# Performance work log

Hardware: AMD Instinct MI355X
Metric: run time of the kernel (lower is better)

Reference implementation:

```python
import jax, jax.numpy as jnp
import numpy as np
from jax import lax

T = 16        # in_length
E = 32        # input_embedding_size_d
H = 64        # encoder_size
NG = 32       # vehicles per scene group
G = 1024      # number of scene groups
N = G * NG    # total vehicles
C = 3         # class_num

leaky = lambda x: jax.nn.leaky_relu(x, 0.1)

def _gru_final(x_seq, Wih, Whh, bih, bhh):
    # x_seq: (T, N, E). PyTorch GRU gate order: r, z, n. Returns final hidden (N, H).
    def step(h, x):
        gx = x @ Wih.T + bih
        gh = h @ Whh.T + bhh
        xr, xz, xn = jnp.split(gx, 3, axis=-1)
        hr, hz, hn = jnp.split(gh, 3, axis=-1)
        r = jax.nn.sigmoid(xr + hr)
        z = jax.nn.sigmoid(xz + hz)
        ng = jnp.tanh(xn + r * hn)
        return (1.0 - z) * ng + z * h, None
    h0 = jnp.zeros((x_seq.shape[1], Whh.shape[1]), x_seq.dtype)
    hT, _ = lax.scan(step, h0, x_seq)
    return hT

def setup_inputs() -> dict:
    key = jax.random.key(0)
    ks = jax.random.split(key, 24)
    def rn(k, shape, fan):
        return jax.random.normal(k, shape, jnp.float32) * np.float32(1.0 / np.sqrt(fan))
    inp = {}
    inp["scene"] = jax.random.normal(ks[0], (N, 2 * T), jnp.float32)
    inp["condition"] = jax.random.randint(ks[1], (N,), 0, C, jnp.int32)
    inp["hero_pos_index"] = jax.random.randint(ks[2], (G,), 0, N, jnp.int32)
    inp["nbrs_pos_index"] = jax.random.randint(ks[3], (N,), 0, N, jnp.int32)
    inp["index_div"] = jnp.arange(N, dtype=jnp.int32).reshape(G, NG)
    # ip_emb_d: Linear(2, E)
    inp["W_emb"] = rn(ks[4], (2, E), 2)
    inp["b_emb"] = jnp.zeros((E,), jnp.float32)
    # forward / backward GRUs (weight_ih: (3H,E), weight_hh: (3H,H))
    inp["Wih_f"] = rn(ks[5], (3 * H, E), E); inp["Whh_f"] = rn(ks[6], (3 * H, H), H)
    inp["bih_f"] = jnp.zeros((3 * H,), jnp.float32); inp["bhh_f"] = jnp.zeros((3 * H,), jnp.float32)
    inp["Wih_b"] = rn(ks[7], (3 * H, E), E); inp["Whh_b"] = rn(ks[8], (3 * H, H), H)
    inp["bih_b"] = jnp.zeros((3 * H,), jnp.float32); inp["bhh_b"] = jnp.zeros((3 * H,), jnp.float32)
    # mlp: Linear(H, H//2)
    inp["Wm"] = rn(ks[9], (H, H // 2), H); inp["bm"] = jnp.zeros((H // 2,), jnp.float32)
    # spatial_mlp: Linear(2T, H) -> Linear(H, H//2)
    inp["Ws1"] = rn(ks[10], (2 * T, H), 2 * T); inp["bs1"] = jnp.zeros((H,), jnp.float32)
    inp["Ws2"] = rn(ks[11], (H, H // 2), H); inp["bs2"] = jnp.zeros((H // 2,), jnp.float32)
    # op_d: Linear(H, H//4) -> Linear(H//4, C)
    inp["Wo1"] = rn(ks[12], (H, H // 4), H); inp["bo1"] = jnp.zeros((H // 4,), jnp.float32)
    inp["Wo2"] = rn(ks[13], (H // 4, C), H // 4); inp["bo2"] = jnp.zeros((C,), jnp.float32)
    return inp

def reference(scene, condition, hero_pos_index, nbrs_pos_index, index_div,
              W_emb, b_emb, Wih_f, Whh_f, bih_f, bhh_f, Wih_b, Whh_b, bih_b, bhh_b,
              Wm, bm, Ws1, bs1, Ws2, bs2, Wo1, bo1, Wo2, bo2):
    n_total = scene.shape[0]
    # scene.view(-1,2,T).permute(2,0,1) -> (T, N, 2)
    scene_t = scene.reshape(n_total, 2, T).transpose(2, 0, 1)
    emb = leaky(scene_t @ W_emb + b_emb)                 # (T, N, E)
    h_f = _gru_final(emb, Wih_f, Whh_f, bih_f, bhh_f)    # (N, H)
    h_b = _gru_final(emb[::-1], Wih_b, Whh_b, bih_b, bhh_b)
    seq_enc = leaky(((h_f + h_b) * 0.5) @ Wm + bm)       # (N, H//2)
    # pairwise relative features within each group: rel[g, j, i] = x_i - x_j
    feat_g = scene[index_div]                            # (G, n, 2T); row layout == permute(1,2,0).view(-1,2T)
    rel = feat_g[:, None, :, :] - feat_g[:, :, None, :]  # (G, n, n, 2T)
    enc = leaky(leaky(rel @ Ws1 + bs1) @ Ws2 + bs2)      # (G, n, n, H//2)
    # diagonal pairs (i==j) are dropped in the original; subtract mlp(0) then divide by n-1
    zero_enc = leaky(leaky(bs1) @ Ws2 + bs2)             # (H//2,)
    n_grp = index_div.shape[1]
    pooled = (enc.sum(axis=2) - zero_enc) / (n_grp - 1)  # (G, n, H//2)
    pooled = pooled.reshape(n_total, -1)                 # group-concat order == vehicle order (arange groups)
    full_enc = jnp.concatenate([seq_enc, pooled], axis=1)  # (N, H)
    x_logit = leaky(full_enc @ Wo1 + bo1) @ Wo2 + bo2      # (N, C)
    return x_logit, full_enc
```

## Files before the change

### kernel.cpp

```cpp
#include <hip/hip_runtime.h>
#include <hip/hip_bf16.h>

#define TT 16
#define EE 32
#define HH 64
#define NGRP 32
#define CC 3

typedef __attribute__((ext_vector_type(8))) short short8;
typedef __attribute__((ext_vector_type(4))) float floatx4;

#define MFMA16(a, b, c) __builtin_amdgcn_mfma_f32_16x16x32_bf16((a), (b), (c), 0, 0, 0)

__device__ __forceinline__ float leakyf(float x) { return fmaxf(x, 0.1f * x); }
__device__ __forceinline__ float sigmoidf_fast(float x) {
    return __builtin_amdgcn_rcpf(1.0f + __expf(-x));
}
__device__ __forceinline__ float tanhf_fast(float x) {
    return 1.0f - 2.0f * __builtin_amdgcn_rcpf(__expf(2.0f * x) + 1.0f);
}
__device__ __forceinline__ short f2bf(float x) {
    unsigned u = __float_as_uint(x);
    return (short)((u + 0x7FFFu + ((u >> 16) & 1u)) >> 16);
}
__device__ __forceinline__ float bf2f(short s) {
    return __uint_as_float(((unsigned)(unsigned short)s) << 16);
}
__device__ __forceinline__ short8 ld8bf(const float* __restrict__ p) {
    const float4 a = *(const float4*)p;
    const float4 b = *(const float4*)(p + 4);
    short8 v;
    v[0] = f2bf(a.x); v[1] = f2bf(a.y); v[2] = f2bf(a.z); v[3] = f2bf(a.w);
    v[4] = f2bf(b.x); v[5] = f2bf(b.y); v[6] = f2bf(b.z); v[7] = f2bf(b.w);
    return v;
}

__global__ __launch_bounds__(512, 6) void gru_mfma_kernel(
    const float* __restrict__ scene,
    const float* __restrict__ W_emb, const float* __restrict__ b_emb,
    const float* __restrict__ Wih_f, const float* __restrict__ Whh_f,
    const float* __restrict__ bih_f, const float* __restrict__ bhh_f,
    const float* __restrict__ Wih_b, const float* __restrict__ Whh_b,
    const float* __restrict__ bih_b, const float* __restrict__ bhh_b,
    const float* __restrict__ Wm, const float* __restrict__ bm,
    float* __restrict__ full_enc)
{
    __shared__ __align__(16) short Xall[16 * 2 * 64 * 8];
    __shared__ __align__(16) short Hf[2 * 2 * 2 * 64 * 8];

    const int tid  = threadIdx.x;
    const int lane = tid & 63;
    const int w    = __builtin_amdgcn_readfirstlane(tid >> 6);
    const int dir  = w >> 2;
    const int wd   = w & 3;
    const int cc   = lane & 15;
    const int quad = lane >> 4;
    const int vbase = blockIdx.x * 32;
    const int j    = wd * 16 + cc;
    const int ks_w = j >> 5;
    const int qa_w = (j >> 3) & 3;
    const int ii_w = j & 7;

    {
        const int t   = tid >> 5;
        const int veh = tid & 31;
        const int n   = vbase + veh;
        const float xs = scene[n * 32 + t];
        const float ys = scene[n * 32 + 16 + t];
        const int mt = veh >> 4;
        const int m  = veh & 15;
        #pragma unroll
        for (int q = 0; q < 4; ++q) {
            short8 v;
            #pragma unroll
            for (int i2 = 0; i2 < 8; ++i2) {
                const int e = q * 8 + i2;
                v[i2] = f2bf(leakyf(fmaf(xs, W_emb[e], fmaf(ys, W_emb[EE + e], b_emb[e]))));
            }
            *(short8*)&Xall[(((t * 2 + mt) * 64) + q * 16 + m) * 8] = v;
        }
        const short8 z8 = {0, 0, 0, 0, 0, 0, 0, 0};
        *(short8*)&Hf[tid * 8] = z8;
    }

    const float* Wih = dir ? Wih_b : Wih_f;
    const float* Whh = dir ? Whh_b : Whh_f;
    const float* bih = dir ? bih_b : bih_f;
    const float* bhh = dir ? bhh_b : bhh_f;
    const int k0 = quad * 8;
    const short8 Br0  = ld8bf(Whh + (j      ) * 64 + k0);
    const short8 Br1  = ld8bf(Whh + (j      ) * 64 + 32 + k0);
    const short8 Br2  = ld8bf(Wih + (j      ) * 32 + k0);
    const short8 Bz0  = ld8bf(Whh + (j +  64) * 64 + k0);
    const short8 Bz1  = ld8bf(Whh + (j +  64) * 64 + 32 + k0);
    const short8 Bz2  = ld8bf(Wih + (j +  64) * 32 + k0);
    const short8 Bhn0 = ld8bf(Whh + (j + 128) * 64 + k0);
    const short8 Bhn1 = ld8bf(Whh + (j + 128) * 64 + 32 + k0);
    const short8 Bxn  = ld8bf(Wih + (j + 128) * 32 + k0);
    const float b_r  = bih[j] + bhh[j];
    const float b_z  = bih[j + 64] + bhh[j + 64];
    const float b_xn = bih[j + 128];
    const float b_hn = bhh[j + 128];

    float h_reg[8];
    #pragma unroll
    for (int i = 0; i < 8; ++i) h_reg[i] = 0.0f;

    short* HfD = &Hf[dir * (2 * 2 * 64 * 8)];
    __syncthreads();

    #pragma unroll 1
    for (int s = 0; s < TT; ++s) {
        const int t = dir ? (TT - 1 - s) : s;
        #pragma unroll
        for (int mt = 0; mt < 2; ++mt) {
            const short8 Ah0 = *(const short8*)&HfD[((0 * 2 + mt) * 64 + lane) * 8];
            const short8 Ah1 = *(const short8*)&HfD[((1 * 2 + mt) * 64 + lane) * 8];
            const short8 Axx = *(const short8*)&Xall[((t * 2 + mt) * 64 + lane) * 8];
            const floatx4 z4 = {0.f, 0.f, 0.f, 0.f};
            const floatx4 ar  = MFMA16(Axx, Br2, MFMA16(Ah1, Br1, MFMA16(Ah0, Br0, z4)));
            const floatx4 az  = MFMA16(Axx, Bz2, MFMA16(Ah1, Bz1, MFMA16(Ah0, Bz0, z4)));
            const floatx4 ahn = MFMA16(Ah1, Bhn1, MFMA16(Ah0, Bhn0, z4));
            const floatx4 axn = MFMA16(Axx, Bxn, z4);
            #pragma unroll
            for (int r = 0; r < 4; ++r) {
                const float rr = sigmoidf_fast(ar[r] + b_r);
                const float zz = sigmoidf_fast(az[r] + b_z);
                const float ng = tanhf_fast(fmaf(rr, ahn[r] + b_hn, axn[r] + b_xn));
                const float h0 = h_reg[mt * 4 + r];
                h_reg[mt * 4 + r] = fmaf(zz, h0 - ng, ng);
            }
        }
        __syncthreads();
        #pragma unroll
        for (int mt = 0; mt < 2; ++mt) {
            #pragma unroll
            for (int r = 0; r < 4; ++r) {
                const int la = qa_w * 16 + (quad * 4 + r);
                HfD[((ks_w * 2 + mt) * 64 + la) * 8 + ii_w] = f2bf(h_reg[mt * 4 + r]);
            }
        }
        __syncthreads();
    }

    if (w < 4) {
        const int nt   = w >> 1;
        const int mt_e = w & 1;
        const int n_col = nt * 16 + cc;
        short8 Bm0, Bm1;
        #pragma unroll
        for (int i = 0; i < 8; ++i) {
            Bm0[i] = f2bf(Wm[(     quad * 8 + i) * 32 + n_col]);
            Bm1[i] = f2bf(Wm[(32 + quad * 8 + i) * 32 + n_col]);
        }
        short8 A0, A1;
        #pragma unroll
        for (int ks = 0; ks < 2; ++ks) {
            const short8 F = *(const short8*)&Hf[(((0 * 2 + ks) * 2 + mt_e) * 64 + lane) * 8];
            const short8 B = *(const short8*)&Hf[(((1 * 2 + ks) * 2 + mt_e) * 64 + lane) * 8];
            #pragma unroll
            for (int i = 0; i < 8; ++i) {
                const short v = f2bf(0.5f * (bf2f(F[i]) + bf2f(B[i])));
                if (ks == 0) A0[i] = v; else A1[i] = v;
            }
        }
        const floatx4 z4 = {0.f, 0.f, 0.f, 0.f};
        const floatx4 acc = MFMA16(A1, Bm1, MFMA16(A0, Bm0, z4));
        const float bmn = bm[n_col];
        #pragma unroll
        for (int r = 0; r < 4; ++r) {
            const int veh = mt_e * 16 + quad * 4 + r;
            full_enc[(vbase + veh) * HH + n_col] = leakyf(acc[r] + bmn);
        }
    }
}

__global__ __launch_bounds__(256, 4) void spatial_mfma_kernel(
    const float* __restrict__ scene, const int* __restrict__ index_div,
    const float* __restrict__ Ws1, const float* __restrict__ bs1,
    const float* __restrict__ Ws2, const float* __restrict__ bs2,
    float* __restrict__ full_enc)
{
    __shared__ float sfeat[NGRP][33];
    __shared__ float su[NGRP][68];
    __shared__ float szero[32];

    const int g    = blockIdx.x;
    const int tid  = threadIdx.x;
    const int lane = tid & 63;
    const int w    = __builtin_amdgcn_readfirstlane(tid >> 6);
    const int cc   = lane & 15;
    const int quad = lane >> 4;

    {
        const int v  = tid >> 3;
        const int c0 = (tid & 7) * 4;
        const int n  = index_div[g * NGRP + v];
        const float4 f4 = *(const float4*)(scene + n * (2 * TT) + c0);
        sfeat[v][c0 + 0] = f4.x; sfeat[v][c0 + 1] = f4.y;
        sfeat[v][c0 + 2] = f4.z; sfeat[v][c0 + 3] = f4.w;
    }
    __syncthreads();

    {
        const int v  = tid >> 3;
        const int d0 = (tid & 7) * 8;
        float acc[8];
        #pragma unroll
        for (int i = 0; i < 8; ++i) acc[i] = 0.0f;
        #pragma unroll
        for (int e = 0; e < EE; ++e) {
            const float f = sfeat[v][e];
            const float4 w0 = *(const float4*)&Ws1[e * 64 + d0];
            const float4 w1 = *(const float4*)&Ws1[e * 64 + d0 + 4];
            acc[0] = fmaf(f, w0.x, acc[0]); acc[1] = fmaf(f, w0.y, acc[1]);
            acc[2] = fmaf(f, w0.z, acc[2]); acc[3] = fmaf(f, w0.w, acc[3]);
            acc[4] = fmaf(f, w1.x, acc[4]); acc[5] = fmaf(f, w1.y, acc[5]);
            acc[6] = fmaf(f, w1.z, acc[6]); acc[7] = fmaf(f, w1.w, acc[7]);
        }
        #pragma unroll
        for (int i = 0; i < 8; ++i) su[v][d0 + i] = acc[i];
    }
    if (tid < 32) {
        float zs = bs2[tid];
        #pragma unroll
        for (int d = 0; d < HH; ++d) zs = fmaf(leakyf(bs1[d]), Ws2[d * 32 + tid], zs);
        szero[tid] = leakyf(zs);
    }

    short8 Bw00, Bw01, Bw10, Bw11;
    #pragma unroll
    for (int i = 0; i < 8; ++i) {
        Bw00[i] = f2bf(Ws2[(     quad * 8 + i) * 32 + cc]);
        Bw01[i] = f2bf(Ws2[(32 + quad * 8 + i) * 32 + cc]);
        Bw10[i] = f2bf(Ws2[(     quad * 8 + i) * 32 + 16 + cc]);
        Bw11[i] = f2bf(Ws2[(32 + quad * 8 + i) * 32 + 16 + cc]);
    }
    float bsq0[8], bsq1[8];
    #pragma unroll
    for (int i = 0; i < 8; ++i) {
        bsq0[i] = bs1[quad * 8 + i];
        bsq1[i] = bs1[32 + quad * 8 + i];
    }
    const float bs2c0 = bs2[cc], bs2c1 = bs2[16 + cc];
    __syncthreads();

    #pragma unroll 2
    for (int jj = 0; jj < 8; ++jj) {
        const int jrow = w * 8 + jj;
        float vj0[8], vj1[8];
        #pragma unroll
        for (int i = 0; i < 8; ++i) {
            vj0[i] = su[jrow][quad * 8 + i] - bsq0[i];
            vj1[i] = su[jrow][32 + quad * 8 + i] - bsq1[i];
        }
        float acc0 = 0.0f, acc1 = 0.0f;
        #pragma unroll
        for (int it = 0; it < 2; ++it) {
            const int irow = it * 16 + cc;
            const float4 p0 = *(const float4*)&su[irow][quad * 8];
            const float4 p1 = *(const float4*)&su[irow][quad * 8 + 4];
            const float4 p2 = *(const float4*)&su[irow][32 + quad * 8];
            const float4 p3 = *(const float4*)&su[irow][32 + quad * 8 + 4];
            short8 A0, A1;
            A0[0] = f2bf(leakyf(p0.x - vj0[0])); A0[1] = f2bf(leakyf(p0.y - vj0[1]));
            A0[2] = f2bf(leakyf(p0.z - vj0[2])); A0[3] = f2bf(leakyf(p0.w - vj0[3]));
            A0[4] = f2bf(leakyf(p1.x - vj0[4])); A0[5] = f2bf(leakyf(p1.y - vj0[5]));
            A0[6] = f2bf(leakyf(p1.z - vj0[6])); A0[7] = f2bf(leakyf(p1.w - vj0[7]));
            A1[0] = f2bf(leakyf(p2.x - vj1[0])); A1[1] = f2bf(leakyf(p2.y - vj1[1]));
            A1[2] = f2bf(leakyf(p2.z - vj1[2])); A1[3] = f2bf(leakyf(p2.w - vj1[3]));
            A1[4] = f2bf(leakyf(p3.x - vj1[4])); A1[5] = f2bf(leakyf(p3.y - vj1[5]));
            A1[6] = f2bf(leakyf(p3.z - vj1[6])); A1[7] = f2bf(leakyf(p3.w - vj1[7]));
            const floatx4 z4 = {0.f, 0.f, 0.f, 0.f};
            const floatx4 D0 = MFMA16(A1, Bw01, MFMA16(A0, Bw00, z4));
            const floatx4 D1 = MFMA16(A1, Bw11, MFMA16(A0, Bw10, z4));
            #pragma unroll
            for (int r = 0; r < 4; ++r) {
                acc0 += leakyf(D0[r] + bs2c0);
                acc1 += leakyf(D1[r] + bs2c1);
            }
        }
        acc0 += __shfl_xor(acc0, 16, 64); acc0 += __shfl_xor(acc0, 32, 64);
        acc1 += __shfl_xor(acc1, 16, 64); acc1 += __shfl_xor(acc1, 32, 64);
        const int row = g * NGRP + jrow;
        if (quad == 0)
            full_enc[row * HH + 32 + cc] = (acc0 - szero[cc]) * (1.0f / 31.0f);
        else if (quad == 1)
            full_enc[row * HH + 48 + cc] = (acc1 - szero[16 + cc]) * (1.0f / 31.0f);
    }
}

__global__ __launch_bounds__(64) void head_kernel(
    const float* __restrict__ full_enc,
    const float* __restrict__ Wo1, const float* __restrict__ bo1,
    const float* __restrict__ Wo2, const float* __restrict__ bo2,
    float* __restrict__ out)
{
    const int n = blockIdx.x * 64 + threadIdx.x;
    float t1[16];
    #pragma unroll
    for (int m = 0; m < 16; ++m) t1[m] = bo1[m];
    const float4* fe4 = (const float4*)(full_enc + n * HH);
    #pragma unroll
    for (int k4 = 0; k4 < 16; ++k4) {
        const float4 f = fe4[k4];
        const float fv[4] = {f.x, f.y, f.z, f.w};
        #pragma unroll
        for (int u = 0; u < 4; ++u) {
            const int k = k4 * 4 + u;
            #pragma unroll
            for (int m = 0; m < 16; ++m) t1[m] = fmaf(fv[u], Wo1[k * 16 + m], t1[m]);
        }
    }
    float l0 = bo2[0], l1 = bo2[1], l2 = bo2[2];
    #pragma unroll
    for (int m = 0; m < 16; ++m) {
        const float a = leakyf(t1[m]);
        l0 = fmaf(a, Wo2[m * 3 + 0], l0);
        l1 = fmaf(a, Wo2[m * 3 + 1], l1);
        l2 = fmaf(a, Wo2[m * 3 + 2], l2);
    }
    out[n * 3 + 0] = l0;
    out[n * 3 + 1] = l1;
    out[n * 3 + 2] = l2;
}

extern "C" void kernel_launch(void* const* d_in, const int* in_sizes, int n_in,
                              void* d_out, int out_size, void* d_ws, size_t ws_size,
                              hipStream_t stream) {
    const float* scene     = (const float*)d_in[0];
    const int*   index_div = (const int*)d_in[4];
    const float* W_emb = (const float*)d_in[5];
    const float* b_emb = (const float*)d_in[6];
    const float* Wih_f = (const float*)d_in[7];
    const float* Whh_f = (const float*)d_in[8];
    const float* bih_f = (const float*)d_in[9];
    const float* bhh_f = (const float*)d_in[10];
    const float* Wih_b = (const float*)d_in[11];
    const float* Whh_b = (const float*)d_in[12];
    const float* bih_b = (const float*)d_in[13];
    const float* bhh_b = (const float*)d_in[14];
    const float* Wm  = (const float*)d_in[15];
    const float* bm  = (const float*)d_in[16];
    const float* Ws1 = (const float*)d_in[17];
    const float* bs1 = (const float*)d_in[18];
    const float* Ws2 = (const float*)d_in[19];
    const float* bs2 = (const float*)d_in[20];
    const float* Wo1 = (const float*)d_in[21];
    const float* bo1 = (const float*)d_in[22];
    const float* Wo2 = (const float*)d_in[23];
    const float* bo2 = (const float*)d_in[24];

    const int N = in_sizes[0] / (2 * TT);
    const int G = in_sizes[4] / NGRP;

    float* out      = (float*)d_out;
    float* full_enc = out + (size_t)N * CC;

    gru_mfma_kernel<<<dim3(N / 32), dim3(512), 0, stream>>>(
        scene, W_emb, b_emb, Wih_f, Whh_f, bih_f, bhh_f,
        Wih_b, Whh_b, bih_b, bhh_b, Wm, bm, full_enc);

    spatial_mfma_kernel<<<dim3(G), dim3(256), 0, stream>>>(
        scene, index_div, Ws1, bs1, Ws2, bs2, full_enc);

    head_kernel<<<dim3(N / 64), dim3(64), 0, stream>>>(
        full_enc, Wo1, bo1, Wo2, bo2, out);
}
```

Baseline: 226.3 us.

## Double-buffer GRU state, compute embeddings per step, fuse head into spatial kernel

The GRU kernel now computes each timestep's input embedding on the fly into a double-buffered LDS tile and ping-pongs the hidden-state buffer, so each step needs one barrier instead of two. It also folds the gate biases into the MFMA accumulator init and uses cheaper round-half-up bf16 conversion. The output head is fused into the spatial kernel, which reads the GRU half of full_enc and keeps the pooled half in LDS, removing a launch and a global round trip. The risks are higher LDS use per block and changed bf16 rounding. The spatial kernel also assumes that group g covers contiguous vehicles g*32 to g*32+31 (arange index_div).

```diff
diff --git a/kernel.cpp b/kernel.cpp
--- a/kernel.cpp
+++ b/kernel.cpp
@@ -8,6 +8,7 @@
 #define CC 3
 
 typedef __attribute__((ext_vector_type(8))) short short8;
+typedef __attribute__((ext_vector_type(4))) short short4v;
 typedef __attribute__((ext_vector_type(4))) float floatx4;
 
 #define MFMA16(a, b, c) __builtin_amdgcn_mfma_f32_16x16x32_bf16((a), (b), (c), 0, 0, 0)
@@ -22,6 +23,9 @@
 __device__ __forceinline__ short f2bf(float x) {
     unsigned u = __float_as_uint(x);
     return (short)((u + 0x7FFFu + ((u >> 16) & 1u)) >> 16);
+}
+__device__ __forceinline__ short f2bf_h(float x) {
+    return (short)((__float_as_uint(x) + 0x8000u) >> 16);
 }
 __device__ __forceinline__ float bf2f(short s) {
     return __uint_as_float(((unsigned)(unsigned short)s) << 16);
@@ -45,8 +49,9 @@
     const float* __restrict__ Wm, const float* __restrict__ bm,
     float* __restrict__ full_enc)
 {
-    __shared__ __align__(16) short Xall[16 * 2 * 64 * 8];
-    __shared__ __align__(16) short Hf[2 * 2 * 2 * 64 * 8];
+    __shared__ float sscene[32][33];
+    __shared__ __align__(16) short Xb[2 * 2 * 2 * 64 * 8];
+    __shared__ __align__(16) short Hf[2 * 2 * 2 * 2 * 64 * 8];
 
     const int tid  = threadIdx.x;
     const int lane = tid & 63;
@@ -61,26 +66,41 @@
     const int qa_w = (j >> 3) & 3;
     const int ii_w = j & 7;
 
+    for (int idx = tid; idx < 1024; idx += 512) {
+        const int v = idx >> 5, c = idx & 31;
+        sscene[c][v] = scene[(vbase + v) * 32 + c];
+    }
     {
-        const int t   = tid >> 5;
-        const int veh = tid & 31;
-        const int n   = vbase + veh;
-        const float xs = scene[n * 32 + t];
-        const float ys = scene[n * 32 + 16 + t];
-        const int mt = veh >> 4;
-        const int m  = veh & 15;
-        #pragma unroll
-        for (int q = 0; q < 4; ++q) {
-            short8 v;
-            #pragma unroll
-            for (int i2 = 0; i2 < 8; ++i2) {
-                const int e = q * 8 + i2;
-                v[i2] = f2bf(leakyf(fmaf(xs, W_emb[e], fmaf(ys, W_emb[EE + e], b_emb[e]))));
-            }
-            *(short8*)&Xall[(((t * 2 + mt) * 64) + q * 16 + m) * 8] = v;
-        }
         const short8 z8 = {0, 0, 0, 0, 0, 0, 0, 0};
-        *(short8*)&Hf[tid * 8] = z8;
+        *(short8*)&Hf[(tid >> 8) * 4096 + (tid & 255) * 8] = z8;
+    }
+
+    const int l     = tid & 255;
+    const int veh_x = l & 31;
+    const int q2    = l >> 5;
+    const int e0    = q2 * 4;
+    const int mtx   = veh_x >> 4;
+    const int mx    = veh_x & 15;
+    const int chx   = e0 >> 3;
+    const int i0x   = e0 & 7;
+    float w0e[4], w1e[4], bbe[4];
+    #pragma unroll
+    for (int d = 0; d < 4; ++d) {
+        w0e[d] = W_emb[e0 + d];
+        w1e[d] = W_emb[EE + e0 + d];
+        bbe[d] = b_emb[e0 + d];
+    }
+    const int xoff = dir * 2048 + (mtx * 64 + chx * 16 + mx) * 8 + i0x;
+
+    {
+        const int t0 = dir ? (TT - 1) : 0;
+        const float xs = sscene[t0][veh_x];
+        const float ys = sscene[16 + t0][veh_x];
+        short4v v;
+        #pragma unroll
+        for (int d = 0; d < 4; ++d)
+            v[d] = f2bf_h(leakyf(fmaf(xs, w0e[d], fmaf(ys, w1e[d], bbe[d]))));
+        *(short4v*)&Xb[xoff] = v;
     }
 
     const float* Wih = dir ? Wih_b : Wih_f;
@@ -101,44 +121,58 @@
     const float b_z  = bih[j + 64] + bhh[j + 64];
     const float b_xn = bih[j + 128];
     const float b_hn = bhh[j + 128];
+    const floatx4 c_r  = {b_r,  b_r,  b_r,  b_r };
+    const floatx4 c_z  = {b_z,  b_z,  b_z,  b_z };
+    const floatx4 c_xn = {b_xn, b_xn, b_xn, b_xn};
+    const floatx4 c_hn = {b_hn, b_hn, b_hn, b_hn};
 
     float h_reg[8];
     #pragma unroll
     for (int i = 0; i < 8; ++i) h_reg[i] = 0.0f;
 
-    short* HfD = &Hf[dir * (2 * 2 * 64 * 8)];
     __syncthreads();
 
-    #pragma unroll 1
+    #pragma unroll 2
     for (int s = 0; s < TT; ++s) {
-        const int t = dir ? (TT - 1 - s) : s;
+        const int pb = s & 1, nb = pb ^ 1;
+        const short* HfD = &Hf[(dir * 2 + pb) * 2048];
+        const short* XbD = &Xb[dir * 2048 + pb * 1024];
         #pragma unroll
         for (int mt = 0; mt < 2; ++mt) {
             const short8 Ah0 = *(const short8*)&HfD[((0 * 2 + mt) * 64 + lane) * 8];
             const short8 Ah1 = *(const short8*)&HfD[((1 * 2 + mt) * 64 + lane) * 8];
-            const short8 Axx = *(const short8*)&Xall[((t * 2 + mt) * 64 + lane) * 8];
-            const floatx4 z4 = {0.f, 0.f, 0.f, 0.f};
-            const floatx4 ar  = MFMA16(Axx, Br2, MFMA16(Ah1, Br1, MFMA16(Ah0, Br0, z4)));
-            const floatx4 az  = MFMA16(Axx, Bz2, MFMA16(Ah1, Bz1, MFMA16(Ah0, Bz0, z4)));
-            const floatx4 ahn = MFMA16(Ah1, Bhn1, MFMA16(Ah0, Bhn0, z4));
-            const floatx4 axn = MFMA16(Axx, Bxn, z4);
+            const short8 Axx = *(const short8*)&XbD[(mt * 64 + lane) * 8];
+            const floatx4 ar  = MFMA16(Axx, Br2, MFMA16(Ah1, Br1, MFMA16(Ah0, Br0, c_r)));
+            const floatx4 az  = MFMA16(Axx, Bz2, MFMA16(Ah1, Bz1, MFMA16(Ah0, Bz0, c_z)));
+            const floatx4 ahn = MFMA16(Ah1, Bhn1, MFMA16(Ah0, Bhn0, c_hn));
+            const floatx4 axn = MFMA16(Axx, Bxn, c_xn);
             #pragma unroll
             for (int r = 0; r < 4; ++r) {
-                const float rr = sigmoidf_fast(ar[r] + b_r);
-                const float zz = sigmoidf_fast(az[r] + b_z);
-                const float ng = tanhf_fast(fmaf(rr, ahn[r] + b_hn, axn[r] + b_xn));
+                const float rr = sigmoidf_fast(ar[r]);
+                const float zz = sigmoidf_fast(az[r]);
+                const float ng = tanhf_fast(fmaf(rr, ahn[r], axn[r]));
                 const float h0 = h_reg[mt * 4 + r];
                 h_reg[mt * 4 + r] = fmaf(zz, h0 - ng, ng);
             }
         }
-        __syncthreads();
+        short* HfN = &Hf[(dir * 2 + nb) * 2048];
         #pragma unroll
         for (int mt = 0; mt < 2; ++mt) {
             #pragma unroll
             for (int r = 0; r < 4; ++r) {
                 const int la = qa_w * 16 + (quad * 4 + r);
-                HfD[((ks_w * 2 + mt) * 64 + la) * 8 + ii_w] = f2bf(h_reg[mt * 4 + r]);
+                HfN[((ks_w * 2 + mt) * 64 + la) * 8 + ii_w] = f2bf_h(h_reg[mt * 4 + r]);
             }
+        }
+        if (s + 1 < TT) {
+            const int tn = dir ? (TT - 2 - s) : (s + 1);
+            const float xs = sscene[tn][veh_x];
+            const float ys = sscene[16 + tn][veh_x];
+            short4v v;
+            #pragma unroll
+            for (int d = 0; d < 4; ++d)
+                v[d] = f2bf_h(leakyf(fmaf(xs, w0e[d], fmaf(ys, w1e[d], bbe[d]))));
+            *(short4v*)&Xb[xoff + nb * 1024] = v;
         }
         __syncthreads();
     }
@@ -156,8 +190,8 @@
         short8 A0, A1;
         #pragma unroll
         for (int ks = 0; ks < 2; ++ks) {
-            const short8 F = *(const short8*)&Hf[(((0 * 2 + ks) * 2 + mt_e) * 64 + lane) * 8];
-            const short8 B = *(const short8*)&Hf[(((1 * 2 + ks) * 2 + mt_e) * 64 + lane) * 8];
+            const short8 F = *(const short8*)&Hf[(0 * 2 + 0) * 2048 + ((ks * 2 + mt_e) * 64 + lane) * 8];
+            const short8 B = *(const short8*)&Hf[(1 * 2 + 0) * 2048 + ((ks * 2 + mt_e) * 64 + lane) * 8];
             #pragma unroll
             for (int i = 0; i < 8; ++i) {
                 const short v = f2bf(0.5f * (bf2f(F[i]) + bf2f(B[i])));
@@ -175,14 +209,18 @@
     }
 }
 
-__global__ __launch_bounds__(256, 4) void spatial_mfma_kernel(
+__global__ __launch_bounds__(256, 4) void spatial_head_kernel(
     const float* __restrict__ scene, const int* __restrict__ index_div,
     const float* __restrict__ Ws1, const float* __restrict__ bs1,
     const float* __restrict__ Ws2, const float* __restrict__ bs2,
-    float* __restrict__ full_enc)
+    const float* __restrict__ Wo1, const float* __restrict__ bo1,
+    const float* __restrict__ Wo2, const float* __restrict__ bo2,
+    float* __restrict__ full_enc, float* __restrict__ out)
 {
     __shared__ float sfeat[NGRP][33];
     __shared__ float su[NGRP][68];
+    __shared__ float fe[NGRP][68];
+    __shared__ float swo1[1024];
     __shared__ float szero[32];
 
     const int g    = blockIdx.x;
@@ -199,6 +237,13 @@
         const float4 f4 = *(const float4*)(scene + n * (2 * TT) + c0);
         sfeat[v][c0 + 0] = f4.x; sfeat[v][c0 + 1] = f4.y;
         sfeat[v][c0 + 2] = f4.z; sfeat[v][c0 + 3] = f4.w;
+        if ((tid & 7) < 8 && c0 < 32) {
+            const float4 s4 = *(const float4*)&full_enc[(g * NGRP + v) * HH + c0];
+            fe[v][c0 + 0] = s4.x; fe[v][c0 + 1] = s4.y;
+            fe[v][c0 + 2] = s4.z; fe[v][c0 + 3] = s4.w;
+        }
+        const float4 q4 = *(const float4*)&Wo1[tid * 4];
+        *(float4*)&swo1[tid * 4] = q4;
     }
     __syncthreads();
 
@@ -283,46 +328,47 @@
         acc0 += __shfl_xor(acc0, 16, 64); acc0 += __shfl_xor(acc0, 32, 64);
         acc1 += __shfl_xor(acc1, 16, 64); acc1 += __shfl_xor(acc1, 32, 64);
         const int row = g * NGRP + jrow;
-        if (quad == 0)
-            full_enc[row * HH + 32 + cc] = (acc0 - szero[cc]) * (1.0f / 31.0f);
-        else if (quad == 1)
-            full_enc[row * HH + 48 + cc] = (acc1 - szero[16 + cc]) * (1.0f / 31.0f);
-    }
-}
-
-__global__ __launch_bounds__(64) void head_kernel(
-    const float* __restrict__ full_enc,
-    const float* __restrict__ Wo1, const float* __restrict__ bo1,
-    const float* __restrict__ Wo2, const float* __restrict__ bo2,
-    float* __restrict__ out)
-{
-    const int n = blockIdx.x * 64 + threadIdx.x;
-    float t1[16];
-    #pragma unroll
-    for (int m = 0; m < 16; ++m) t1[m] = bo1[m];
-    const float4* fe4 = (const float4*)(full_enc + n * HH);
-    #pragma unroll
-    for (int k4 = 0; k4 < 16; ++k4) {
-        const float4 f = fe4[k4];
-        const float fv[4] = {f.x, f.y, f.z, f.w};
-        #pragma unroll
-        for (int u = 0; u < 4; ++u) {
-            const int k = k4 * 4 + u;
-            #pragma unroll
-            for (int m = 0; m < 16; ++m) t1[m] = fmaf(fv[u], Wo1[k * 16 + m], t1[m]);
-        }
-    }
-    float l0 = bo2[0], l1 = bo2[1], l2 = bo2[2];
-    #pragma unroll
-    for (int m = 0; m < 16; ++m) {
-        const float a = leakyf(t1[m]);
-        l0 = fmaf(a, Wo2[m * 3 + 0], l0);
-        l1 = fmaf(a, Wo2[m * 3 + 1], l1);
-        l2 = fmaf(a, Wo2[m * 3 + 2], l2);
-    }
-    out[n * 3 + 0] = l0;
-    out[n * 3 + 1] = l1;
-    out[n * 3 + 2] = l2;
+        if (quad == 0) {
+            const float pv = (acc0 - szero[cc]) * (1.0f / 31.0f);
+            full_enc[row * HH + 32 + cc] = pv;
+            fe[jrow][32 + cc] = pv;
+        } else if (quad == 1) {
+            const float pv = (acc1 - szero[16 + cc]) * (1.0f / 31.0f);
+            full_enc[row * HH + 48 + cc] = pv;
+            fe[jrow][48 + cc] = pv;
+        }
+    }
+    __syncthreads();
+
+    {
+        const int veh = tid >> 3;
+        const int p   = tid & 7;
+        const int m0  = p * 2;
+        float a0 = bo1[m0], a1 = bo1[m0 + 1];
+        #pragma unroll
+        for (int k = 0; k < HH; ++k) {
+            const float f = fe[veh][k];
+            const float2 wv = *(const float2*)&swo1[k * 16 + m0];
+            a0 = fmaf(f, wv.x, a0);
+            a1 = fmaf(f, wv.y, a1);
+        }
+        a0 = leakyf(a0); a1 = leakyf(a1);
+        float l0 = fmaf(a0, Wo2[m0 * 3 + 0], a1 * Wo2[(m0 + 1) * 3 + 0]);
+        float l1 = fmaf(a0, Wo2[m0 * 3 + 1], a1 * Wo2[(m0 + 1) * 3 + 1]);
+        float l2 = fmaf(a0, Wo2[m0 * 3 + 2], a1 * Wo2[(m0 + 1) * 3 + 2]);
+        #pragma unroll
+        for (int off = 1; off < 8; off <<= 1) {
+            l0 += __shfl_xor(l0, off, 64);
+            l1 += __shfl_xor(l1, off, 64);
+            l2 += __shfl_xor(l2, off, 64);
+        }
+        if (p == 0) {
+            const int n = g * NGRP + veh;
+            out[n * 3 + 0] = l0 + bo2[0];
+            out[n * 3 + 1] = l1 + bo2[1];
+            out[n * 3 + 2] = l2 + bo2[2];
+        }
+    }
 }
 
 extern "C" void kernel_launch(void* const* d_in, const int* in_sizes, int n_in,
@@ -361,9 +407,7 @@
         scene, W_emb, b_emb, Wih_f, Whh_f, bih_f, bhh_f,
         Wih_b, Whh_b, bih_b, bhh_b, Wm, bm, full_enc);
 
-    spatial_mfma_kernel<<<dim3(G), dim3(256), 0, stream>>>(
-        scene, index_div, Ws1, bs1, Ws2, bs2, full_enc);
-
-    head_kernel<<<dim3(N / 64), dim3(64), 0, stream>>>(
-        full_enc, Wo1, bo1, Wo2, bo2, out);
-}
+    spatial_head_kernel<<<dim3(G), dim3(256), 0, stream>>>(
+        scene, index_div, Ws1, bs1, Ws2, bs2, Wo1, bo1, Wo2, bo2,
+        full_enc, out);
+}
```

Result: slower. 466.7 us (+106.2%).
